# Kernel tuning notes

Measured on AMD Instinct MI355X. Metric: run time of the kernel, lower is better.

## Reference

```python
import jax, jax.numpy as jnp
import numpy as np

GRID_RES = 64
BOUND = 1.2

def _coords():
    lin = jnp.linspace(-BOUND, BOUND, GRID_RES, dtype=jnp.float32)
    gx, gy, gz = jnp.meshgrid(lin, lin, lin, indexing='ij')
    return jnp.stack([gx, gy, gz], axis=-1).reshape(-1, 3)  # (R^3, 3)

def setup_inputs() -> dict:
    key = jax.random.key(0)
    ks = jax.random.split(key, 9)
    B, D, H = 2, 512, 512
    s_in = 1.0 / np.sqrt(D + 3)
    s_h = 1.0 / np.sqrt(H)
    return {
        'cad_latent': jax.random.normal(ks[0], (B, D), jnp.float32),
        'W0': jax.random.normal(ks[1], (D + 3, H), jnp.float32) * s_in,
        'b0': jax.random.normal(ks[2], (H,), jnp.float32) * s_in,
        'W1': jax.random.normal(ks[3], (H, H), jnp.float32) * s_h,
        'b1': jax.random.normal(ks[4], (H,), jnp.float32) * s_h,
        'W2': jax.random.normal(ks[5], (H, H), jnp.float32) * s_h,
        'b2': jax.random.normal(ks[6], (H,), jnp.float32) * s_h,
        'W3': jax.random.normal(ks[7], (H, 1), jnp.float32) * s_h,
        'b3': jax.random.normal(ks[8], (1,), jnp.float32) * s_h,
    }

def reference(cad_latent, W0, b0, W1, b1, W2, b2, W3, b3):
    B, D = cad_latent.shape
    coords = _coords()  # (P, 3), P = R^3
    # First layer: concat([latent, coords]) @ W0 decomposed to avoid
    # materializing the broadcast-concatenated (B, P, D+3) tensor.
    lat_part = cad_latent @ W0[:D]          # (B, H)
    coord_part = coords @ W0[D:]            # (P, H)
    h = jax.nn.silu(lat_part[:, None, :] + coord_part[None, :, :] + b0)  # (B, P, H)
    h = jax.nn.silu(h @ W1 + b1)
    h = jax.nn.silu(h @ W2 + b2)
    sdf = h @ W3 + b3                       # (B, P, 1)
    return sdf.reshape(B, GRID_RES, GRID_RES, GRID_RES)
```

## Files before the change

kernel.cpp:

```cpp
#include <hip/hip_runtime.h>

#define H 512
#define MTILE 64
#define NBLK 8192
#define STEPC (2.4f / 63.0f)

typedef _Float16 half8 __attribute__((ext_vector_type(8)));
typedef _Float16 half4_t __attribute__((ext_vector_type(4)));
typedef float floatx4 __attribute__((ext_vector_type(4)));
typedef float floatx2 __attribute__((ext_vector_type(2)));

__device__ inline float silu_f(float x) {
    return __fdividef(x, 1.0f + __expf(-x));
}

__global__ void prep_latw(const float* __restrict__ lat, const float* __restrict__ W0,
                          const float* __restrict__ b0, float* __restrict__ latw) {
    __shared__ float sl[H];
    const int b = blockIdx.x;
    const int j = threadIdx.x;
    sl[j] = lat[b * H + j];
    __syncthreads();
    float acc = b0[j];
#pragma unroll 8
    for (int d = 0; d < H; ++d) acc += sl[d] * W0[d * H + j];
    latw[b * H + j] = acc;
}

__global__ void prep_w16(const float* __restrict__ W1, const float* __restrict__ W2,
                         _Float16* __restrict__ ws) {
    const int id = blockIdx.x * 512 + threadIdx.x;
    const int l = id >> 18;
    const int rem = id & 0x3FFFF;
    const int k = rem >> 9, n = rem & 511;
    const float w = (l == 0 ? W1 : W2)[rem];
    const int kc = k >> 5, q = (k >> 3) & 3, k0 = k & 7;
    ws[((size_t)((l * 16 + kc) * 4 + q) * 512 + n) * 8 + k0] = (_Float16)w;
}

__global__ __launch_bounds__(512, 4) void mesh_main(
    const float* __restrict__ W0, const float* __restrict__ b1,
    const float* __restrict__ b2, const float* __restrict__ W3,
    const float* __restrict__ b3, const float* __restrict__ latw,
    const _Float16* __restrict__ wsB, float* __restrict__ out) {

    __shared__ _Float16 hbuf2[4096 * 8];
    __shared__ float lwbuf[2 * H];
    __shared__ float partials[8][MTILE];

    const int tid = threadIdx.x;
    const int wave = tid >> 6, lane = tid & 63;
    const int q = lane >> 4, t = lane & 15;
    const int bi = blockIdx.x;
    const int b = bi >> 12;
    const int p0 = (bi & 4095) << 6;
    const float c0 = -1.2f + (float)(p0 >> 12) * STEPC;
    const float c1 = -1.2f + (float)((p0 >> 6) & 63) * STEPC;

    {
        const int j = tid;
        const float lwv = latw[b * H + j]
                        + c0 * W0[(H + 0) * H + j]
                        + c1 * W0[(H + 1) * H + j];
        floatx2 v;
        v[0] = lwv;
        v[1] = W0[(H + 2) * H + j];
        *(floatx2*)&lwbuf[2 * j] = v;
    }
    __syncthreads();

    {
        const float c2v = -1.2f + (float)lane * STEPC;
#pragma unroll
        for (int s = 0; s < 8; ++s) {
            const int g = wave * 8 + s;
            const floatx4* lp = (const floatx4*)&lwbuf[g * 16];
            half8 hv;
#pragma unroll
            for (int i = 0; i < 4; ++i) {
                const floatx4 pv = lp[i];
                hv[2 * i + 0] = (_Float16)silu_f(pv[0] + c2v * pv[1]);
                hv[2 * i + 1] = (_Float16)silu_f(pv[2] + c2v * pv[3]);
            }
            *(half8*)&hbuf2[(g * 64 + lane) * 8] = hv;
        }
    }

    const _Float16* wsl = wsB + ((size_t)q * 512 + wave * 16 + t) * 8;
    const _Float16* hb = hbuf2 + q * 512 + t * 8;

    floatx4 acc[4][4];

    auto zero_acc = [&]() {
#pragma unroll
        for (int mf = 0; mf < 4; ++mf)
#pragma unroll
            for (int nt = 0; nt < 4; ++nt) {
                acc[mf][nt][0] = 0.f; acc[mf][nt][1] = 0.f;
                acc[mf][nt][2] = 0.f; acc[mf][nt][3] = 0.f;
            }
    };

    auto loadB = [&](int l, int kc, half8 (&bf)[4]) {
        const _Float16* p = wsl + (size_t)(l * 16 + kc) * 16384;
#pragma unroll
        for (int nt = 0; nt < 4; ++nt)
            bf[nt] = *(const half8*)(p + nt * 1024);
    };

    auto compute = [&](int kc, half8 (&bf)[4]) {
        half8 a[4];
        const _Float16* hp = hb + kc * 2048;
#pragma unroll
        for (int mf = 0; mf < 4; ++mf)
            a[mf] = *(const half8*)(hp + mf * 128);
#pragma unroll
        for (int nt = 0; nt < 4; ++nt)
#pragma unroll
            for (int mf = 0; mf < 4; ++mf)
                acc[mf][nt] = __builtin_amdgcn_mfma_f32_16x16x32_f16(bf[nt], a[mf], acc[mf][nt], 0, 0, 0);
    };

    auto run_gemm = [&](int l) {
        half8 B0[4], B1[4];
        loadB(l, 0, B0);
#pragma unroll 1
        for (int kc = 0; kc < 16; kc += 2) {
            loadB(l, kc + 1, B1);
            compute(kc, B0);
            loadB(l, (kc + 2) & 15, B0);
            compute(kc + 1, B1);
        }
    };

    zero_acc();
    __syncthreads();
    run_gemm(0);
    __syncthreads();
    {
        const int R0 = (wave >> 1) * 4 + (wave & 1) * 2 + (q >> 1);
        _Float16* wb = hbuf2 + R0 * 512 + t * 8 + (q & 1) * 4;
        floatx4 b1v[4];
#pragma unroll
        for (int nt = 0; nt < 4; ++nt)
            b1v[nt] = *(const floatx4*)&b1[nt * 128 + wave * 16 + q * 4];
#pragma unroll
        for (int mf = 0; mf < 4; ++mf)
#pragma unroll
            for (int nt = 0; nt < 4; ++nt) {
                half4_t hv;
#pragma unroll
                for (int r = 0; r < 4; ++r)
                    hv[r] = (_Float16)silu_f(acc[mf][nt][r] + b1v[nt][r]);
                *(half4_t*)(wb + nt * 8192 + mf * 128) = hv;
            }
    }

    zero_acc();
    __syncthreads();
    run_gemm(1);

    {
        floatx4 b2v[4], w3v[4];
#pragma unroll
        for (int nt = 0; nt < 4; ++nt) {
            b2v[nt] = *(const floatx4*)&b2[nt * 128 + wave * 16 + q * 4];
            w3v[nt] = *(const floatx4*)&W3[nt * 128 + wave * 16 + q * 4];
        }
#pragma unroll
        for (int mf = 0; mf < 4; ++mf) {
            float sum = 0.f;
#pragma unroll
            for (int nt = 0; nt < 4; ++nt)
#pragma unroll
                for (int r = 0; r < 4; ++r)
                    sum += silu_f(acc[mf][nt][r] + b2v[nt][r]) * w3v[nt][r];
            sum += __shfl_xor(sum, 16);
            sum += __shfl_xor(sum, 32);
            if (lane < 16) partials[wave][mf * 16 + t] = sum;
        }
    }
    __syncthreads();
    if (tid < MTILE) {
        float o = b3[0];
#pragma unroll
        for (int w = 0; w < 8; ++w) o += partials[w][tid];
        out[(size_t)bi * MTILE + tid] = o;
    }
}

extern "C" void kernel_launch(void* const* d_in, const int* in_sizes, int n_in,
                              void* d_out, int out_size, void* d_ws, size_t ws_size,
                              hipStream_t stream) {
    const float* lat = (const float*)d_in[0];
    const float* W0  = (const float*)d_in[1];
    const float* b0  = (const float*)d_in[2];
    const float* W1  = (const float*)d_in[3];
    const float* b1  = (const float*)d_in[4];
    const float* W2  = (const float*)d_in[5];
    const float* b2  = (const float*)d_in[6];
    const float* W3  = (const float*)d_in[7];
    const float* b3  = (const float*)d_in[8];
    float* out = (float*)d_out;

    float* latw = (float*)d_ws;
    _Float16* wsB = (_Float16*)((char*)d_ws + 4096);

    prep_latw<<<2, 512, 0, stream>>>(lat, W0, b0, latw);
    prep_w16<<<1024, 512, 0, stream>>>(W1, W2, wsB);
    mesh_main<<<NBLK, 512, 0, stream>>>(W0, b1, b2, W3, b3, latw, wsB, out);
}
```

Before: 811.7 us.

## Stage weight tiles into LDS via async global_load_lds double buffering

Replaces per-wave direct global loads of the fp16 weight fragments with block-cooperative asynchronous global-to-LDS copies into a double buffer. Each weight K-chunk is then read from LDS by all waves, and the first layer-2 chunks are prefetched during the layer-1 epilogue. This cuts redundant global/L2 traffic and hides latency. In exchange it adds 64KB of LDS and two barriers per K step, and lowers the launch-bounds occupancy hint from 4 to 2 blocks.

New measurement: 1.117 ms. 37.6% more time.

```diff
diff --git a/kernel.cpp b/kernel.cpp
--- a/kernel.cpp
+++ b/kernel.cpp
@@ -1,4 +1,5 @@
 #include <hip/hip_runtime.h>
+#include <stdint.h>
 
 #define H 512
 #define MTILE 64
@@ -38,13 +39,14 @@
     ws[((size_t)((l * 16 + kc) * 4 + q) * 512 + n) * 8 + k0] = (_Float16)w;
 }
 
-__global__ __launch_bounds__(512, 4) void mesh_main(
+__global__ __launch_bounds__(512, 2) void mesh_main(
     const float* __restrict__ W0, const float* __restrict__ b1,
     const float* __restrict__ b2, const float* __restrict__ W3,
     const float* __restrict__ b3, const float* __restrict__ latw,
     const _Float16* __restrict__ wsB, float* __restrict__ out) {
 
     __shared__ _Float16 hbuf2[4096 * 8];
+    __shared__ _Float16 bs[2][16384];
     __shared__ float lwbuf[2 * H];
     __shared__ float partials[8][MTILE];
 
@@ -57,6 +59,20 @@
     const float c0 = -1.2f + (float)(p0 >> 12) * STEPC;
     const float c1 = -1.2f + (float)((p0 >> 6) & 63) * STEPC;
 
+    auto stage = [&](int buf, int l, int kc) {
+        const _Float16* src = wsB + ((size_t)(l * 16 + kc) * 16384 + wave * 2048 + lane * 8);
+        _Float16* dst = &bs[buf][wave * 2048];
+#pragma unroll
+        for (int i = 0; i < 4; ++i)
+            __builtin_amdgcn_global_load_lds(
+                (const __attribute__((address_space(1))) void*)(src + i * 512),
+                (__attribute__((address_space(3))) void*)(dst + i * 512),
+                16, 0, 0);
+    };
+
+    stage(0, 0, 0);
+    stage(1, 0, 1);
+
     {
         const int j = tid;
         const float lwv = latw[b * H + j]
@@ -86,8 +102,8 @@
         }
     }
 
-    const _Float16* wsl = wsB + ((size_t)q * 512 + wave * 16 + t) * 8;
     const _Float16* hb = hbuf2 + q * 512 + t * 8;
+    const int boff = q * 4096 + wave * 128 + t * 8;
 
     floatx4 acc[4][4];
 
@@ -101,15 +117,17 @@
             }
     };
 
-    auto loadB = [&](int l, int kc, half8 (&bf)[4]) {
-        const _Float16* p = wsl + (size_t)(l * 16 + kc) * 16384;
+    auto kphase = [&](int l, int kc, int buf, bool vm0, bool restage) {
+        if (vm0) { asm volatile("s_waitcnt vmcnt(0)" ::: "memory"); }
+        else     { asm volatile("s_waitcnt vmcnt(4)" ::: "memory"); }
+        __builtin_amdgcn_sched_barrier(0);
+        __builtin_amdgcn_s_barrier();
+        __builtin_amdgcn_sched_barrier(0);
+        half8 bf[4], a[4];
+        const _Float16* bp = &bs[buf][boff];
 #pragma unroll
         for (int nt = 0; nt < 4; ++nt)
-            bf[nt] = *(const half8*)(p + nt * 1024);
-    };
-
-    auto compute = [&](int kc, half8 (&bf)[4]) {
-        half8 a[4];
+            bf[nt] = *(const half8*)(bp + nt * 1024);
         const _Float16* hp = hb + kc * 2048;
 #pragma unroll
         for (int mf = 0; mf < 4; ++mf)
@@ -119,24 +137,28 @@
 #pragma unroll
             for (int mf = 0; mf < 4; ++mf)
                 acc[mf][nt] = __builtin_amdgcn_mfma_f32_16x16x32_f16(bf[nt], a[mf], acc[mf][nt], 0, 0, 0);
+        __builtin_amdgcn_sched_barrier(0);
+        __builtin_amdgcn_s_barrier();
+        if (restage) stage(buf, l, kc + 2);
     };
 
     auto run_gemm = [&](int l) {
-        half8 B0[4], B1[4];
-        loadB(l, 0, B0);
 #pragma unroll 1
-        for (int kc = 0; kc < 16; kc += 2) {
-            loadB(l, kc + 1, B1);
-            compute(kc, B0);
-            loadB(l, (kc + 2) & 15, B0);
-            compute(kc + 1, B1);
-        }
+        for (int kc = 0; kc < 14; kc += 2) {
+            kphase(l, kc,     0, false, true);
+            kphase(l, kc + 1, 1, false, true);
+        }
+        kphase(l, 14, 0, false, false);
+        kphase(l, 15, 1, true,  false);
     };
 
     zero_acc();
     __syncthreads();
     run_gemm(0);
-    __syncthreads();
+
+    stage(0, 1, 0);
+    stage(1, 1, 1);
+
     {
         const int R0 = (wave >> 1) * 4 + (wave & 1) * 2 + (q >> 1);
         _Float16* wb = hbuf2 + R0 * 512 + t * 8 + (q & 1) * 4;
```

## Switch hidden-layer GEMMs to 32x32x16 MFMA with contiguous per-wave N slices

Applied to the files above, without the earlier changes.

Replaces the 16x16x32 f16 MFMA tiling (4x4 fragments per wave) with 32x32x16 MFMA using 2x2 floatx16 accumulators. Each wave now owns a contiguous 64-column slice of the output. The fp16 weight repacking layout, LDS activation indexing, and epilogue mappings are rewritten to match. The weight prefetch becomes a 4-stage register rotation over 32 K-steps. The intent is fewer A/B fragment loads per FLOP and higher MFMA throughput, at the cost of a different LDS access pattern that may cause bank conflicts.

Measured after the change: 835.8 us. +3.0%, slower.

```diff
diff --git a/kernel.cpp b/kernel.cpp
--- a/kernel.cpp
+++ b/kernel.cpp
@@ -7,6 +7,7 @@
 
 typedef _Float16 half8 __attribute__((ext_vector_type(8)));
 typedef _Float16 half4_t __attribute__((ext_vector_type(4)));
+typedef float floatx16 __attribute__((ext_vector_type(16)));
 typedef float floatx4 __attribute__((ext_vector_type(4)));
 typedef float floatx2 __attribute__((ext_vector_type(2)));
 
@@ -34,8 +35,7 @@
     const int rem = id & 0x3FFFF;
     const int k = rem >> 9, n = rem & 511;
     const float w = (l == 0 ? W1 : W2)[rem];
-    const int kc = k >> 5, q = (k >> 3) & 3, k0 = k & 7;
-    ws[((size_t)((l * 16 + kc) * 4 + q) * 512 + n) * 8 + k0] = (_Float16)w;
+    ws[((size_t)(l * 64 + (k >> 3)) * 512 + n) * 8 + (k & 7)] = (_Float16)w;
 }
 
 __global__ __launch_bounds__(512, 4) void mesh_main(
@@ -50,7 +50,7 @@
 
     const int tid = threadIdx.x;
     const int wave = tid >> 6, lane = tid & 63;
-    const int q = lane >> 4, t = lane & 15;
+    const int lm = lane & 31, hi = lane >> 5;
     const int bi = blockIdx.x;
     const int b = bi >> 12;
     const int p0 = (bi & 4095) << 6;
@@ -86,98 +86,107 @@
         }
     }
 
-    const _Float16* wsl = wsB + ((size_t)q * 512 + wave * 16 + t) * 8;
-    const _Float16* hb = hbuf2 + q * 512 + t * 8;
-
-    floatx4 acc[4][4];
+    const _Float16* hb = hbuf2 + hi * 512 + lm * 8;
+    const _Float16* wsl = wsB + ((size_t)hi * 512 + wave * 64 + lm) * 8;
+
+    floatx16 acc[2][2];
 
     auto zero_acc = [&]() {
 #pragma unroll
-        for (int mf = 0; mf < 4; ++mf)
-#pragma unroll
-            for (int nt = 0; nt < 4; ++nt) {
-                acc[mf][nt][0] = 0.f; acc[mf][nt][1] = 0.f;
-                acc[mf][nt][2] = 0.f; acc[mf][nt][3] = 0.f;
+        for (int mb = 0; mb < 2; ++mb)
+#pragma unroll
+            for (int nt = 0; nt < 2; ++nt)
+#pragma unroll
+                for (int r = 0; r < 16; ++r) acc[mb][nt][r] = 0.f;
+    };
+
+    auto loadW = [&](int l, int ks, half8 (&wf)[2]) {
+        const _Float16* p = wsl + (size_t)(l * 32 + ks) * 8192;
+        wf[0] = *(const half8*)(p);
+        wf[1] = *(const half8*)(p + 256);
+    };
+
+    auto compute = [&](int ks, half8 (&wf)[2]) {
+        half8 a[2];
+        const _Float16* hp = hb + ks * 1024;
+        a[0] = *(const half8*)(hp);
+        a[1] = *(const half8*)(hp + 256);
+#pragma unroll
+        for (int nt = 0; nt < 2; ++nt)
+#pragma unroll
+            for (int mb = 0; mb < 2; ++mb)
+                acc[mb][nt] = __builtin_amdgcn_mfma_f32_32x32x16_f16(wf[nt], a[mb], acc[mb][nt], 0, 0, 0);
+    };
+
+    auto run_gemm = [&](int l) {
+        half8 Wb0[2], Wb1[2], Wb2[2], Wb3[2];
+        loadW(l, 0, Wb0);
+        loadW(l, 1, Wb1);
+#pragma unroll 1
+        for (int ks = 0; ks < 32; ks += 4) {
+            loadW(l, (ks + 2) & 31, Wb2);
+            compute(ks, Wb0);
+            loadW(l, (ks + 3) & 31, Wb3);
+            compute(ks + 1, Wb1);
+            loadW(l, (ks + 4) & 31, Wb0);
+            compute(ks + 2, Wb2);
+            loadW(l, (ks + 5) & 31, Wb1);
+            compute(ks + 3, Wb3);
+        }
+    };
+
+    zero_acc();
+    __syncthreads();
+    run_gemm(0);
+    __syncthreads();
+    {
+        _Float16* wb = hbuf2 + (wave * 8) * 512 + lm * 8 + hi * 4;
+        floatx4 b1v[2][4];
+#pragma unroll
+        for (int nt = 0; nt < 2; ++nt)
+#pragma unroll
+            for (int g = 0; g < 4; ++g)
+                b1v[nt][g] = *(const floatx4*)&b1[wave * 64 + nt * 32 + g * 8 + hi * 4];
+#pragma unroll
+        for (int mb = 0; mb < 2; ++mb)
+#pragma unroll
+            for (int nt = 0; nt < 2; ++nt)
+#pragma unroll
+                for (int g = 0; g < 4; ++g) {
+                    half4_t hv;
+#pragma unroll
+                    for (int j = 0; j < 4; ++j)
+                        hv[j] = (_Float16)silu_f(acc[mb][nt][g * 4 + j] + b1v[nt][g][j]);
+                    *(half4_t*)(wb + (nt * 4 + g) * 512 + mb * 256) = hv;
+                }
+    }
+
+    zero_acc();
+    __syncthreads();
+    run_gemm(1);
+
+    {
+        floatx4 b2v[2][4], w3v[2][4];
+#pragma unroll
+        for (int nt = 0; nt < 2; ++nt)
+#pragma unroll
+            for (int g = 0; g < 4; ++g) {
+                const int n0 = wave * 64 + nt * 32 + g * 8 + hi * 4;
+                b2v[nt][g] = *(const floatx4*)&b2[n0];
+                w3v[nt][g] = *(const floatx4*)&W3[n0];
             }
-    };
-
-    auto loadB = [&](int l, int kc, half8 (&bf)[4]) {
-        const _Float16* p = wsl + (size_t)(l * 16 + kc) * 16384;
-#pragma unroll
-        for (int nt = 0; nt < 4; ++nt)
-            bf[nt] = *(const half8*)(p + nt * 1024);
-    };
-
-    auto compute = [&](int kc, half8 (&bf)[4]) {
-        half8 a[4];
-        const _Float16* hp = hb + kc * 2048;
-#pragma unroll
-        for (int mf = 0; mf < 4; ++mf)
-            a[mf] = *(const half8*)(hp + mf * 128);
-#pragma unroll
-        for (int nt = 0; nt < 4; ++nt)
-#pragma unroll
-            for (int mf = 0; mf < 4; ++mf)
-                acc[mf][nt] = __builtin_amdgcn_mfma_f32_16x16x32_f16(bf[nt], a[mf], acc[mf][nt], 0, 0, 0);
-    };
-
-    auto run_gemm = [&](int l) {
-        half8 B0[4], B1[4];
-        loadB(l, 0, B0);
-#pragma unroll 1
-        for (int kc = 0; kc < 16; kc += 2) {
-            loadB(l, kc + 1, B1);
-            compute(kc, B0);
-            loadB(l, (kc + 2) & 15, B0);
-            compute(kc + 1, B1);
-        }
-    };
-
-    zero_acc();
-    __syncthreads();
-    run_gemm(0);
-    __syncthreads();
-    {
-        const int R0 = (wave >> 1) * 4 + (wave & 1) * 2 + (q >> 1);
-        _Float16* wb = hbuf2 + R0 * 512 + t * 8 + (q & 1) * 4;
-        floatx4 b1v[4];
-#pragma unroll
-        for (int nt = 0; nt < 4; ++nt)
-            b1v[nt] = *(const floatx4*)&b1[nt * 128 + wave * 16 + q * 4];
-#pragma unroll
-        for (int mf = 0; mf < 4; ++mf)
-#pragma unroll
-            for (int nt = 0; nt < 4; ++nt) {
-                half4_t hv;
-#pragma unroll
-                for (int r = 0; r < 4; ++r)
-                    hv[r] = (_Float16)silu_f(acc[mf][nt][r] + b1v[nt][r]);
-                *(half4_t*)(wb + nt * 8192 + mf * 128) = hv;
-            }
-    }
-
-    zero_acc();
-    __syncthreads();
-    run_gemm(1);
-
-    {
-        floatx4 b2v[4], w3v[4];
-#pragma unroll
-        for (int nt = 0; nt < 4; ++nt) {
-            b2v[nt] = *(const floatx4*)&b2[nt * 128 + wave * 16 + q * 4];
-            w3v[nt] = *(const floatx4*)&W3[nt * 128 + wave * 16 + q * 4];
-        }
-#pragma unroll
-        for (int mf = 0; mf < 4; ++mf) {
+#pragma unroll
+        for (int mb = 0; mb < 2; ++mb) {
             float sum = 0.f;
 #pragma unroll
-            for (int nt = 0; nt < 4; ++nt)
-#pragma unroll
-                for (int r = 0; r < 4; ++r)
-                    sum += silu_f(acc[mf][nt][r] + b2v[nt][r]) * w3v[nt][r];
-            sum += __shfl_xor(sum, 16);
+            for (int nt = 0; nt < 2; ++nt)
+#pragma unroll
+                for (int g = 0; g < 4; ++g)
+#pragma unroll
+                    for (int j = 0; j < 4; ++j)
+                        sum += silu_f(acc[mb][nt][g * 4 + j] + b2v[nt][g][j]) * w3v[nt][g][j];
             sum += __shfl_xor(sum, 32);
-            if (lane < 16) partials[wave][mf * 16 + t] = sum;
+            if (hi == 0) partials[wave][mb * 32 + lm] = sum;
         }
     }
     __syncthreads();
```
